# Performance work log

Measured on AMD Instinct MI355X. Metric: run time of the kernel, lower is better.

Reference implementation:

```python
import jax, jax.numpy as jnp
import numpy as np
from jax import lax

WINDOW = 11  # window_size from init
C1 = 0.01 ** 2
C2 = 0.03 ** 2


def _avg_pool(x, w=WINDOW):
    # matches torch avg_pool2d(kernel=w, stride=1, padding=w//2, count_include_pad=True)
    p = w // 2
    s = lax.reduce_window(x, 0.0, lax.add,
                          window_dimensions=(1, 1, w, w),
                          window_strides=(1, 1, 1, 1),
                          padding=((0, 0), (0, 0), (p, p), (p, p)))
    return s / (w * w)


def setup_inputs() -> dict:
    key = jax.random.key(0)
    k1, k2 = jax.random.split(key)
    shape = (32, 3, 512, 512)
    pred = jax.random.uniform(k1, shape, dtype=jnp.float32)
    target = jax.random.uniform(k2, shape, dtype=jnp.float32)
    return {"pred": pred, "target": target}


def reference(pred, target):
    mu1 = _avg_pool(pred)
    mu2 = _avg_pool(target)
    mu1_sq = mu1 * mu1
    mu2_sq = mu2 * mu2
    mu1_mu2 = mu1 * mu2
    sigma1_sq = _avg_pool(pred * pred) - mu1_sq
    sigma2_sq = _avg_pool(target * target) - mu2_sq
    sigma12 = _avg_pool(pred * target) - mu1_mu2
    ssim_map = ((2 * mu1_mu2 + C1) * (2 * sigma12 + C2)) / ((mu1_sq + mu2_sq + C1) * (sigma1_sq + sigma2_sq + C2))
    return 1.0 - jnp.mean(ssim_map)  # size_average=True
```

## Files before the change

### kernel.cpp

```cpp
#include <hip/hip_runtime.h>


#define IMGW 512
#define IMGPIX (IMGW * IMGW)
#define CH 32
#define NCHUNK 16
#define NBUF 48
#define RING (NBUF * 64)
#define PBLOCKS 768

__global__ __launch_bounds__(256, 3)
void ssim_strip(const float* __restrict__ pred,
                const float* __restrict__ target,
                double* __restrict__ accum)
{
    __shared__ float4 sH[RING];
    __shared__ double wpart[4];

    const int tid = threadIdx.x;
    const int img = blockIdx.x >> 3, bx = blockIdx.x & 7;
    const float* __restrict__ p = pred   + (size_t)img * IMGPIX;
    const float* __restrict__ t = target + (size_t)img * IMGPIX;

    const int j    = tid >> 3;
    const int xr   = tid & 7;
    const int xbase = bx * 64 + xr * 8;
    const int lane = tid & 63;
    const int w    = tid >> 6;
    const int lx   = lane ^ ((lane >> 3) & 7);
    const bool edge = (bx == 0) || (bx == 7);

    int goff[6]; float xm[6];
#pragma unroll
    for (int c2 = 0; c2 < 6; ++c2) {
        const int gx = xbase - 8 + 4 * c2;
        xm[c2] = ((unsigned)gx < (unsigned)IMGW) ? 1.f : 0.f;
        goff[c2] = gx < 0 ? 0 : (gx > IMGW - 4 ? IMGW - 4 : gx);
    }

    float fp[24], ft[24];

    auto apply_edge = [&]() {
#pragma unroll
        for (int c2 = 0; c2 < 6; ++c2) {
            const float m = xm[c2];
#pragma unroll
            for (int q = 0; q < 4; ++q) { fp[4*c2+q] *= m; ft[4*c2+q] *= m; }
        }
    };

    auto loadF = [&](const float* pr, const float* tr) {
#pragma unroll
        for (int c2 = 0; c2 < 6; ++c2) {
            const float4 pv = *(const float4*)(pr + goff[c2]);
            const float4 tv = *(const float4*)(tr + goff[c2]);
            fp[4*c2+0]=pv.x; fp[4*c2+1]=pv.y; fp[4*c2+2]=pv.z; fp[4*c2+3]=pv.w;
            ft[4*c2+0]=tv.x; ft[4*c2+1]=tv.y; ft[4*c2+2]=tv.z; ft[4*c2+3]=tv.w;
        }
        if (edge) apply_edge();
    };

    auto loadG = [&](int r) {
        if ((unsigned)r < (unsigned)IMGW) {
            loadF(p + (size_t)r * IMGW, t + (size_t)r * IMGW);
        } else {
#pragma unroll
            for (int i = 0; i < 24; ++i) { fp[i] = 0.f; ft[i] = 0.f; }
        }
    };

    auto stageB = [&](int sl) {
        float s1=0.f, s2=0.f, s3=0.f, s4=0.f;
#pragma unroll
        for (int i = 3; i <= 13; ++i) {
            s1 += fp[i]; s2 += ft[i];
            s3 += fp[i]*fp[i] + ft[i]*ft[i];
            s4 += fp[i]*ft[i];
        }
        const int wbi = (sl << 6) + (xr << 3);
#pragma unroll
        for (int k = 0; k < 8; ++k) {
            if (k) {
                const int a = k + 13, b = k + 2;
                s1 += fp[a] - fp[b];
                s2 += ft[a] - ft[b];
                s3 += (fp[a]*fp[a] + ft[a]*ft[a]) - (fp[b]*fp[b] + ft[b]*ft[b]);
                s4 += fp[a]*ft[a] - fp[b]*ft[b];
            }
            sH[wbi + (k ^ xr)] = make_float4(s1, s2, s3, s4);
        }
    };

    auto barrier_lds = [&]() {
        asm volatile("s_waitcnt lgkmcnt(0)" ::: "memory");
        __builtin_amdgcn_s_barrier();
        asm volatile("" ::: "memory");
    };

    loadG(-5 + j);
    stageB(j);
    if (tid < 80) {
        loadF(p + (size_t)(27 + j) * IMGW, t + (size_t)(27 + j) * IMGW);
        stageB(32 + j);
    }
    barrier_lds();

    const float inv = 1.0f / 121.0f;
    const float C1 = 1e-4f, C2 = 9e-4f;

    const float* pf = p + (size_t)(37 + j) * IMGW;
    const float* tf = t + (size_t)(37 + j) * IMGW;
    int wb = 42 + j; if (wb >= NBUF) wb -= NBUF;
    int cs = 8 * w;
    double acc = 0.0;

    for (int c = 0; c < NCHUNK; ++c) {
        if (c < 14)       { loadF(pf, tf); pf += CH * IMGW; tf += CH * IMGW; }
        else if (c == 14) { loadG(485 + j); }
        __builtin_amdgcn_sched_barrier(0);

        int ri = (cs << 6) + lx;
        float4 rr[8];
        float4 S = {0.f, 0.f, 0.f, 0.f};
#pragma unroll
        for (int i = 0; i < 10; ++i) {
            const float4 a = sH[ri];
            if (i < 8) rr[i] = a;
            S.x += a.x; S.y += a.y; S.z += a.z; S.w += a.w;
            ri += 64; if (ri >= RING) ri -= RING;
        }
        float tl = 0.f;
#pragma unroll
        for (int k = 0; k < 8; ++k) {
            const float4 nw = sH[ri];
            ri += 64; if (ri >= RING) ri -= RING;
            const float W1 = S.x + nw.x, W2 = S.y + nw.y;
            const float W3 = S.z + nw.z, W4 = S.w + nw.w;
            S.x = W1 - rr[k].x; S.y = W2 - rr[k].y;
            S.z = W3 - rr[k].z; S.w = W4 - rr[k].w;

            const float mu1 = W1*inv, mu2 = W2*inv;
            const float E3  = W3*inv, E12 = W4*inv;
            const float mu11 = mu1*mu1, mu22 = mu2*mu2, mu12 = mu1*mu2;
            const float num = (2.f*mu12 + C1) * (2.f*(E12 - mu12) + C2);
            const float den = (mu11 + mu22 + C1) * ((E3 - mu11 - mu22) + C2);
            float rdn = __builtin_amdgcn_rcpf(den);
            rdn = rdn * __builtin_fmaf(-den, rdn, 2.0f);
            tl += num * rdn;
        }
        acc += (double)tl;
        cs += CH; if (cs >= NBUF) cs -= NBUF;

        barrier_lds();
        if (c < NCHUNK - 1) {
            stageB(wb);
            wb += CH; if (wb >= NBUF) wb -= NBUF;
        }
        barrier_lds();
    }

#pragma unroll
    for (int off = 32; off > 0; off >>= 1)
        acc += __shfl_down(acc, off, 64);
    if (lane == 0) wpart[w] = acc;
    __syncthreads();
    if (tid == 0)
        atomicAdd(accum, wpart[0] + wpart[1] + wpart[2] + wpart[3]);
}

__global__ void ssim_finalize(const double* __restrict__ accum,
                              float* __restrict__ out) {
    const double n = 25165824.0;
    out[0] = (float)(1.0 - accum[0] / n);
}

extern "C" void kernel_launch(void* const* d_in, const int* in_sizes, int n_in,
                              void* d_out, int out_size, void* d_ws, size_t ws_size,
                              hipStream_t stream) {
    const float* pred   = (const float*)d_in[0];
    const float* target = (const float*)d_in[1];
    float* out = (float*)d_out;
    double* accum = (double*)d_ws;

    hipMemsetAsync(d_ws, 0, sizeof(double), stream);

    ssim_strip<<<dim3(PBLOCKS), dim3(256), 0, stream>>>(pred, target, accum);
    ssim_finalize<<<1, 1, 0, stream>>>(accum, out);
}
```

Measured before the change: 259.3 us.

## Split each image column strip into two row halves with smaller LDS ring

Doubles the grid by giving each block half an image's rows (256) instead of all 512, shrinking the per-chunk row count and the LDS ring from 48 to 32 slots so more blocks fit per CU (launch bounds raised to 5). Only half the threads now load and stage horizontal sums, while all threads consume vertical sums. The register cache of old rows is dropped in favour of re-reading from LDS, and ring wrapping now uses a power-of-two mask. The aim is better occupancy and latency hiding, at the cost of extra halo rows loaded per block, idle stager lanes and more LDS reads.

```diff
diff --git a/kernel.cpp b/kernel.cpp
--- a/kernel.cpp
+++ b/kernel.cpp
@@ -3,89 +3,89 @@
 
 #define IMGW 512
 #define IMGPIX (IMGW * IMGW)
-#define CH 32
+#define CH 16
 #define NCHUNK 16
-#define NBUF 48
-#define RING (NBUF * 64)
-#define PBLOCKS 768
+#define NBUF 32
+#define RINGF4 (NBUF * 64)
+#define RMASK (RINGF4 - 1)
+#define NBLK 1536
 
-__global__ __launch_bounds__(256, 3)
+__global__ __launch_bounds__(256, 5)
 void ssim_strip(const float* __restrict__ pred,
                 const float* __restrict__ target,
                 double* __restrict__ accum)
 {
-    __shared__ float4 sH[RING];
-    __shared__ double wpart[4];
+    __shared__ float4 sH[RINGF4];
 
     const int tid = threadIdx.x;
-    const int img = blockIdx.x >> 3, bx = blockIdx.x & 7;
+    const int b = blockIdx.x;
+    const int bx = b & 7, hh = (b >> 3) & 1, img = b >> 4;
     const float* __restrict__ p = pred   + (size_t)img * IMGPIX;
     const float* __restrict__ t = target + (size_t)img * IMGPIX;
+    const int ybase = hh << 8;
 
-    const int j    = tid >> 3;
-    const int xr   = tid & 7;
-    const int xbase = bx * 64 + xr * 8;
+    const bool stager = tid < 128;
+    const int j2 = tid >> 3;
+    const int xr = tid & 7;
+    const int xoff = bx * 64 + xr * 8 - 8;
+    const bool edge = (bx == 0) | (bx == 7);
     const int lane = tid & 63;
-    const int w    = tid >> 6;
-    const int lx   = lane ^ ((lane >> 3) & 7);
-    const bool edge = (bx == 0) || (bx == 7);
-
-    int goff[6]; float xm[6];
-#pragma unroll
-    for (int c2 = 0; c2 < 6; ++c2) {
-        const int gx = xbase - 8 + 4 * c2;
-        xm[c2] = ((unsigned)gx < (unsigned)IMGW) ? 1.f : 0.f;
-        goff[c2] = gx < 0 ? 0 : (gx > IMGW - 4 ? IMGW - 4 : gx);
-    }
+    const int w = tid >> 6;
+    const int lx = lane ^ ((lane >> 3) & 7);
 
     float fp[24], ft[24];
 
-    auto apply_edge = [&]() {
+    auto loadRow = [&](int r) {
+        const bool rok = (unsigned)r < (unsigned)IMGW;
+        if (rok) {
+            const float* pr = p + (size_t)r * IMGW;
+            const float* tr = t + (size_t)r * IMGW;
+            if (!edge) {
 #pragma unroll
-        for (int c2 = 0; c2 < 6; ++c2) {
-            const float m = xm[c2];
+                for (int c2 = 0; c2 < 6; ++c2) {
+                    const float4 pv = *(const float4*)(pr + xoff + 4 * c2);
+                    const float4 tv = *(const float4*)(tr + xoff + 4 * c2);
+                    fp[4*c2+0]=pv.x; fp[4*c2+1]=pv.y; fp[4*c2+2]=pv.z; fp[4*c2+3]=pv.w;
+                    ft[4*c2+0]=tv.x; ft[4*c2+1]=tv.y; ft[4*c2+2]=tv.z; ft[4*c2+3]=tv.w;
+                }
+            } else {
 #pragma unroll
-            for (int q = 0; q < 4; ++q) { fp[4*c2+q] *= m; ft[4*c2+q] *= m; }
-        }
-    };
-
-    auto loadF = [&](const float* pr, const float* tr) {
-#pragma unroll
-        for (int c2 = 0; c2 < 6; ++c2) {
-            const float4 pv = *(const float4*)(pr + goff[c2]);
-            const float4 tv = *(const float4*)(tr + goff[c2]);
-            fp[4*c2+0]=pv.x; fp[4*c2+1]=pv.y; fp[4*c2+2]=pv.z; fp[4*c2+3]=pv.w;
-            ft[4*c2+0]=tv.x; ft[4*c2+1]=tv.y; ft[4*c2+2]=tv.z; ft[4*c2+3]=tv.w;
-        }
-        if (edge) apply_edge();
-    };
-
-    auto loadG = [&](int r) {
-        if ((unsigned)r < (unsigned)IMGW) {
-            loadF(p + (size_t)r * IMGW, t + (size_t)r * IMGW);
+                for (int c2 = 0; c2 < 6; ++c2) {
+                    const int gx = xoff + 4 * c2;
+                    const bool ok = (unsigned)gx < (unsigned)IMGW;
+                    const int gxc = gx < 0 ? 0 : (gx > IMGW - 4 ? IMGW - 4 : gx);
+                    const float4 pv = *(const float4*)(pr + gxc);
+                    const float4 tv = *(const float4*)(tr + gxc);
+                    const float m = ok ? 1.f : 0.f;
+                    fp[4*c2+0]=pv.x*m; fp[4*c2+1]=pv.y*m;
+                    fp[4*c2+2]=pv.z*m; fp[4*c2+3]=pv.w*m;
+                    ft[4*c2+0]=tv.x*m; ft[4*c2+1]=tv.y*m;
+                    ft[4*c2+2]=tv.z*m; ft[4*c2+3]=tv.w*m;
+                }
+            }
         } else {
 #pragma unroll
             for (int i = 0; i < 24; ++i) { fp[i] = 0.f; ft[i] = 0.f; }
         }
     };
 
-    auto stageB = [&](int sl) {
-        float s1=0.f, s2=0.f, s3=0.f, s4=0.f;
+    auto stageB = [&](int sb) {
+        float s1 = 0.f, s2 = 0.f, s3 = 0.f, s4 = 0.f;
 #pragma unroll
         for (int i = 3; i <= 13; ++i) {
             s1 += fp[i]; s2 += ft[i];
             s3 += fp[i]*fp[i] + ft[i]*ft[i];
             s4 += fp[i]*ft[i];
         }
-        const int wbi = (sl << 6) + (xr << 3);
+        const int wbi = sb + (xr << 3);
 #pragma unroll
         for (int k = 0; k < 8; ++k) {
             if (k) {
-                const int a = k + 13, b = k + 2;
-                s1 += fp[a] - fp[b];
-                s2 += ft[a] - ft[b];
-                s3 += (fp[a]*fp[a] + ft[a]*ft[a]) - (fp[b]*fp[b] + ft[b]*ft[b]);
-                s4 += fp[a]*ft[a] - fp[b]*ft[b];
+                const int a = k + 13, bb = k + 2;
+                s1 += fp[a] - fp[bb];
+                s2 += ft[a] - ft[bb];
+                s3 += (fp[a]*fp[a] + ft[a]*ft[a]) - (fp[bb]*fp[bb] + ft[bb]*ft[bb]);
+                s4 += fp[a]*ft[a] - fp[bb]*ft[bb];
             }
             sH[wbi + (k ^ xr)] = make_float4(s1, s2, s3, s4);
         }
@@ -97,50 +97,47 @@
         asm volatile("" ::: "memory");
     };
 
-    loadG(-5 + j);
-    stageB(j);
-    if (tid < 80) {
-        loadF(p + (size_t)(27 + j) * IMGW, t + (size_t)(27 + j) * IMGW);
-        stageB(32 + j);
+    if (stager) {
+        loadRow(ybase - 5 + j2);
+        stageB(j2 << 6);
+        if (tid < 80) {
+            loadRow(ybase + 11 + j2);
+            stageB((16 + j2) << 6);
+        }
     }
     barrier_lds();
 
     const float inv = 1.0f / 121.0f;
     const float C1 = 1e-4f, C2 = 9e-4f;
 
-    const float* pf = p + (size_t)(37 + j) * IMGW;
-    const float* tf = t + (size_t)(37 + j) * IMGW;
-    int wb = 42 + j; if (wb >= NBUF) wb -= NBUF;
-    int cs = 8 * w;
+    int cri = (4 * w) << 6;
+    int sb  = ((26 + j2) & 31) << 6;
     double acc = 0.0;
 
     for (int c = 0; c < NCHUNK; ++c) {
-        if (c < 14)       { loadF(pf, tf); pf += CH * IMGW; tf += CH * IMGW; }
-        else if (c == 14) { loadG(485 + j); }
+        if (stager && c < NCHUNK - 1) loadRow(ybase + 16 * c + 21 + j2);
         __builtin_amdgcn_sched_barrier(0);
 
-        int ri = (cs << 6) + lx;
-        float4 rr[8];
+        int ri = cri + lx;
+        int rj = ri;
         float4 S = {0.f, 0.f, 0.f, 0.f};
 #pragma unroll
         for (int i = 0; i < 10; ++i) {
-            const float4 a = sH[ri];
-            if (i < 8) rr[i] = a;
+            const float4 a = sH[ri]; ri = (ri + 64) & RMASK;
             S.x += a.x; S.y += a.y; S.z += a.z; S.w += a.w;
-            ri += 64; if (ri >= RING) ri -= RING;
         }
         float tl = 0.f;
 #pragma unroll
-        for (int k = 0; k < 8; ++k) {
-            const float4 nw = sH[ri];
-            ri += 64; if (ri >= RING) ri -= RING;
+        for (int k = 0; k < 4; ++k) {
+            const float4 nw = sH[ri]; ri = (ri + 64) & RMASK;
             const float W1 = S.x + nw.x, W2 = S.y + nw.y;
             const float W3 = S.z + nw.z, W4 = S.w + nw.w;
-            S.x = W1 - rr[k].x; S.y = W2 - rr[k].y;
-            S.z = W3 - rr[k].z; S.w = W4 - rr[k].w;
+            const float4 old = sH[rj]; rj = (rj + 64) & RMASK;
+            S.x = W1 - old.x; S.y = W2 - old.y;
+            S.z = W3 - old.z; S.w = W4 - old.w;
 
-            const float mu1 = W1*inv, mu2 = W2*inv;
-            const float E3  = W3*inv, E12 = W4*inv;
+            const float mu1 = W1 * inv, mu2 = W2 * inv;
+            const float E3  = W3 * inv, E12 = W4 * inv;
             const float mu11 = mu1*mu1, mu22 = mu2*mu2, mu12 = mu1*mu2;
             const float num = (2.f*mu12 + C1) * (2.f*(E12 - mu12) + C2);
             const float den = (mu11 + mu22 + C1) * ((E3 - mu11 - mu22) + C2);
@@ -149,12 +146,12 @@
             tl += num * rdn;
         }
         acc += (double)tl;
-        cs += CH; if (cs >= NBUF) cs -= NBUF;
+        cri = (cri + CH * 64) & RMASK;
 
         barrier_lds();
-        if (c < NCHUNK - 1) {
-            stageB(wb);
-            wb += CH; if (wb >= NBUF) wb -= NBUF;
+        if (stager && c < NCHUNK - 1) {
+            stageB(sb);
+            sb = (sb + CH * 64) & RMASK;
         }
         barrier_lds();
     }
@@ -162,10 +159,13 @@
 #pragma unroll
     for (int off = 32; off > 0; off >>= 1)
         acc += __shfl_down(acc, off, 64);
-    if (lane == 0) wpart[w] = acc;
     __syncthreads();
-    if (tid == 0)
-        atomicAdd(accum, wpart[0] + wpart[1] + wpart[2] + wpart[3]);
+    if (lane == 0) ((double*)sH)[w] = acc;
+    __syncthreads();
+    if (tid == 0) {
+        const double* red = (const double*)sH;
+        atomicAdd(accum, red[0] + red[1] + red[2] + red[3]);
+    }
 }
 
 __global__ void ssim_finalize(const double* __restrict__ accum,
@@ -184,6 +184,6 @@
 
     hipMemsetAsync(d_ws, 0, sizeof(double), stream);
 
-    ssim_strip<<<dim3(PBLOCKS), dim3(256), 0, stream>>>(pred, target, accum);
+    ssim_strip<<<dim3(NBLK), dim3(256), 0, stream>>>(pred, target, accum);
     ssim_finalize<<<1, 1, 0, stream>>>(accum, out);
 }
```

Result: slower. 681.8 us (+163.0%).
